# Kernel tuning notes

Hardware: AMD Instinct MI355X
Metric: run time of the kernel (lower is better)

Reference implementation:

```python
import jax, jax.numpy as jnp
import numpy as np

B, D = 8192, 4096  # batch, flattened feature dim
RATIO = 0.2


def setup_inputs() -> dict:
    key = jax.random.key(0)
    x = jax.random.normal(key, (B, D), dtype=jnp.float32)
    k = int(np.ceil(RATIO * D))  # 820, static for lax.top_k
    return {"x": x, "k": k}


def reference(x, k):
    # k-Winners-Take-All: per row, keep values >= k-th largest, zero the rest.
    kth_largest = jax.lax.top_k(x, k)[0][:, -1]  # [B]
    return jnp.where(x < kth_largest[:, None], 0.0, x)
```

## Files before the change

### kernel.cpp

```cpp
#include <hip/hip_runtime.h>
#include <stdint.h>

#define D_DIM   4096
#define THREADS 256

__device__ __forceinline__ int wave_reduce_add(int v) {
    #pragma unroll
    for (int m = 32; m >= 1; m >>= 1) v += __shfl_xor(v, m, 64);
    return v;
}
__device__ __forceinline__ uint32_t wave_reduce_min(uint32_t v) {
    #pragma unroll
    for (int m = 32; m >= 1; m >>= 1) {
        uint32_t o = (uint32_t)__shfl_xor((int)v, m, 64);
        v = (o < v) ? o : v;
    }
    return v;
}
__device__ __forceinline__ uint32_t wave_reduce_max(uint32_t v) {
    #pragma unroll
    for (int m = 32; m >= 1; m >>= 1) {
        uint32_t o = (uint32_t)__shfl_xor((int)v, m, 64);
        v = (o > v) ? o : v;
    }
    return v;
}

__global__ __launch_bounds__(THREADS, 4)
void kwta_kernel(const float* __restrict__ x, const int* __restrict__ kptr,
                 float* __restrict__ out) {
    const int row  = blockIdx.x;
    const int t    = threadIdx.x;
    const int wid  = t >> 6;
    const int lane = t & 63;
    const size_t base = (size_t)row * D_DIM;
    const float4* __restrict__ xr = reinterpret_cast<const float4*>(x + base);
    float4* __restrict__ orow     = reinterpret_cast<float4*>(out + base);
    const int k = kptr[0];

    uint32_t u[16];
    #pragma unroll
    for (int j = 0; j < 4; ++j) {
        float4 v = xr[t + j * THREADS];
        uint32_t b[4] = { __float_as_uint(v.x), __float_as_uint(v.y),
                          __float_as_uint(v.z), __float_as_uint(v.w) };
        #pragma unroll
        for (int e = 0; e < 4; ++e) {
            uint32_t f = b[e];
            u[j * 4 + e] = ((int32_t)f < 0) ? ~f : (f | 0x80000000u);
        }
    }

    uint32_t mn = 0xFFFFFFFFu, mx = 0u;
    #pragma unroll
    for (int e = 0; e < 16; ++e) {
        mn = (u[e] < mn) ? u[e] : mn;
        mx = (u[e] > mx) ? u[e] : mx;
    }
    mn = wave_reduce_min(mn);
    mx = wave_reduce_max(mx);

    __shared__ uint32_t smn[4], smx[4];
    __shared__ int      scnt[4];
    if (lane == 0) { smn[wid] = mn; smx[wid] = mx; }
    __syncthreads();
    uint32_t lo = smn[0]; lo = (smn[1] < lo) ? smn[1] : lo;
             lo = (smn[2] < lo) ? smn[2] : lo; lo = (smn[3] < lo) ? smn[3] : lo;
    uint32_t hi = smx[0]; hi = (smx[1] > hi) ? smx[1] : hi;
             hi = (smx[2] > hi) ? smx[2] : hi; hi = (smx[3] > hi) ? smx[3] : hi;

    #pragma unroll 1
    while (lo < hi) {
        uint32_t diff = hi - lo;
        uint32_t mid  = lo + (diff >> 1) + (diff & 1u);
        int c = 0;
        #pragma unroll
        for (int e = 0; e < 16; ++e) c += (u[e] >= mid) ? 1 : 0;
        c = wave_reduce_add(c);
        __syncthreads();
        if (lane == 0) scnt[wid] = c;
        __syncthreads();
        int total = scnt[0] + scnt[1] + scnt[2] + scnt[3];
        if (total >= k) lo = mid; else hi = mid - 1u;
    }

    const uint32_t thr = lo;
    #pragma unroll
    for (int j = 0; j < 4; ++j) {
        float4 o;
        float* po = &o.x;
        #pragma unroll
        for (int e = 0; e < 4; ++e) {
            uint32_t uu = u[j * 4 + e];
            uint32_t f  = (uu & 0x80000000u) ? (uu ^ 0x80000000u) : ~uu;
            po[e] = (uu >= thr) ? __uint_as_float(f) : 0.0f;
        }
        orow[t + j * THREADS] = o;
    }
}

extern "C" void kernel_launch(void* const* d_in, const int* in_sizes, int n_in,
                              void* d_out, int out_size, void* d_ws, size_t ws_size,
                              hipStream_t stream) {
    const float* x    = (const float*)d_in[0];
    const int*   kptr = (const int*)d_in[1];
    float*       out  = (float*)d_out;
    const int rows = out_size / D_DIM;
    kwta_kernel<<<rows, THREADS, 0, stream>>>(x, kptr, out);
}
```

Baseline: 261.2 us.

## Assign one wavefront per row and count with ballot/popcount instead of block barriers

Each 64-lane wavefront now owns a full row (64 values per lane), so the per-row binary-search threshold is found without shared memory or __syncthreads. The per-iteration count uses ballot plus popcount on each element instead of a shuffle reduction followed by two block barriers. This removes the roughly 32 barrier round-trips per row. In exchange, register use rises to 64 values per lane, which may lower occupancy, and there are 64 ballots per search step.

```diff
diff --git a/kernel.cpp b/kernel.cpp
--- a/kernel.cpp
+++ b/kernel.cpp
@@ -1,14 +1,9 @@
 #include <hip/hip_runtime.h>
 #include <stdint.h>
 
-#define D_DIM   4096
-#define THREADS 256
+#define D_DIM          4096
+#define ROWS_PER_BLOCK 4
 
-__device__ __forceinline__ int wave_reduce_add(int v) {
-    #pragma unroll
-    for (int m = 32; m >= 1; m >>= 1) v += __shfl_xor(v, m, 64);
-    return v;
-}
 __device__ __forceinline__ uint32_t wave_reduce_min(uint32_t v) {
     #pragma unroll
     for (int m = 32; m >= 1; m >>= 1) {
@@ -26,22 +21,21 @@
     return v;
 }
 
-__global__ __launch_bounds__(THREADS, 4)
+__global__ __launch_bounds__(256)
 void kwta_kernel(const float* __restrict__ x, const int* __restrict__ kptr,
                  float* __restrict__ out) {
-    const int row  = blockIdx.x;
-    const int t    = threadIdx.x;
-    const int wid  = t >> 6;
-    const int lane = t & 63;
+    const int wid  = threadIdx.x >> 6;
+    const int lane = threadIdx.x & 63;
+    const int row  = blockIdx.x * ROWS_PER_BLOCK + wid;
     const size_t base = (size_t)row * D_DIM;
     const float4* __restrict__ xr = reinterpret_cast<const float4*>(x + base);
     float4* __restrict__ orow     = reinterpret_cast<float4*>(out + base);
     const int k = kptr[0];
 
-    uint32_t u[16];
+    uint32_t u[64];
     #pragma unroll
-    for (int j = 0; j < 4; ++j) {
-        float4 v = xr[t + j * THREADS];
+    for (int j = 0; j < 16; ++j) {
+        float4 v = xr[lane + j * 64];
         uint32_t b[4] = { __float_as_uint(v.x), __float_as_uint(v.y),
                           __float_as_uint(v.z), __float_as_uint(v.w) };
         #pragma unroll
@@ -53,21 +47,12 @@
 
     uint32_t mn = 0xFFFFFFFFu, mx = 0u;
     #pragma unroll
-    for (int e = 0; e < 16; ++e) {
+    for (int e = 0; e < 64; ++e) {
         mn = (u[e] < mn) ? u[e] : mn;
         mx = (u[e] > mx) ? u[e] : mx;
     }
-    mn = wave_reduce_min(mn);
-    mx = wave_reduce_max(mx);
-
-    __shared__ uint32_t smn[4], smx[4];
-    __shared__ int      scnt[4];
-    if (lane == 0) { smn[wid] = mn; smx[wid] = mx; }
-    __syncthreads();
-    uint32_t lo = smn[0]; lo = (smn[1] < lo) ? smn[1] : lo;
-             lo = (smn[2] < lo) ? smn[2] : lo; lo = (smn[3] < lo) ? smn[3] : lo;
-    uint32_t hi = smx[0]; hi = (smx[1] > hi) ? smx[1] : hi;
-             hi = (smx[2] > hi) ? smx[2] : hi; hi = (smx[3] > hi) ? smx[3] : hi;
+    uint32_t lo = wave_reduce_min(mn);
+    uint32_t hi = wave_reduce_max(mx);
 
     #pragma unroll 1
     while (lo < hi) {
@@ -75,18 +60,14 @@
         uint32_t mid  = lo + (diff >> 1) + (diff & 1u);
         int c = 0;
         #pragma unroll
-        for (int e = 0; e < 16; ++e) c += (u[e] >= mid) ? 1 : 0;
-        c = wave_reduce_add(c);
-        __syncthreads();
-        if (lane == 0) scnt[wid] = c;
-        __syncthreads();
-        int total = scnt[0] + scnt[1] + scnt[2] + scnt[3];
-        if (total >= k) lo = mid; else hi = mid - 1u;
+        for (int e = 0; e < 64; ++e)
+            c += (int)__popcll(__ballot(u[e] >= mid));
+        if (c >= k) lo = mid; else hi = mid - 1u;
     }
 
     const uint32_t thr = lo;
     #pragma unroll
-    for (int j = 0; j < 4; ++j) {
+    for (int j = 0; j < 16; ++j) {
         float4 o;
         float* po = &o.x;
         #pragma unroll
@@ -95,7 +76,7 @@
             uint32_t f  = (uu & 0x80000000u) ? (uu ^ 0x80000000u) : ~uu;
             po[e] = (uu >= thr) ? __uint_as_float(f) : 0.0f;
         }
-        orow[t + j * THREADS] = o;
+        orow[lane + j * 64] = o;
     }
 }
 
@@ -105,6 +86,7 @@
     const float* x    = (const float*)d_in[0];
     const int*   kptr = (const int*)d_in[1];
     float*       out  = (float*)d_out;
-    const int rows = out_size / D_DIM;
-    kwta_kernel<<<rows, THREADS, 0, stream>>>(x, kptr, out);
+    const int rows   = out_size / D_DIM;
+    const int blocks = rows / ROWS_PER_BLOCK;
+    kwta_kernel<<<blocks, 256, 0, stream>>>(x, kptr, out);
 }
```

New measurement: 270.6 us. 1.04x slower.

## Replace bisection threshold search with 4-pass 8-bit radix select via LDS histograms

Applied to the files above, without the earlier changes.

Replaces the up-to-32-iteration binary search over the order-preserving uint keys with a 4-level radix select. Each level builds a 256-bin shared-memory histogram of the next 8 bits for elements matching the current prefix, then uses a wave suffix scan to locate the bin containing the k-th largest. This cuts the number of block-wide reductions and barriers from about 32 to 4, at the cost of LDS atomics that may contend when many values share a bin. The launch bounds are also raised to request more resident blocks per CU.

```diff
diff --git a/kernel.cpp b/kernel.cpp
--- a/kernel.cpp
+++ b/kernel.cpp
@@ -4,39 +4,18 @@
 #define D_DIM   4096
 #define THREADS 256
 
-__device__ __forceinline__ int wave_reduce_add(int v) {
-    #pragma unroll
-    for (int m = 32; m >= 1; m >>= 1) v += __shfl_xor(v, m, 64);
-    return v;
-}
-__device__ __forceinline__ uint32_t wave_reduce_min(uint32_t v) {
-    #pragma unroll
-    for (int m = 32; m >= 1; m >>= 1) {
-        uint32_t o = (uint32_t)__shfl_xor((int)v, m, 64);
-        v = (o < v) ? o : v;
-    }
-    return v;
-}
-__device__ __forceinline__ uint32_t wave_reduce_max(uint32_t v) {
-    #pragma unroll
-    for (int m = 32; m >= 1; m >>= 1) {
-        uint32_t o = (uint32_t)__shfl_xor((int)v, m, 64);
-        v = (o > v) ? o : v;
-    }
-    return v;
-}
-
-__global__ __launch_bounds__(THREADS, 4)
+__global__ __launch_bounds__(THREADS, 8)
 void kwta_kernel(const float* __restrict__ x, const int* __restrict__ kptr,
                  float* __restrict__ out) {
+    __shared__ uint32_t hist[2][256];
+
+    const int t    = threadIdx.x;
+    const int lane = t & 63;
     const int row  = blockIdx.x;
-    const int t    = threadIdx.x;
-    const int wid  = t >> 6;
-    const int lane = t & 63;
     const size_t base = (size_t)row * D_DIM;
     const float4* __restrict__ xr = reinterpret_cast<const float4*>(x + base);
     float4* __restrict__ orow     = reinterpret_cast<float4*>(out + base);
-    const int k = kptr[0];
+    int k = kptr[0];
 
     uint32_t u[16];
     #pragma unroll
@@ -51,40 +30,60 @@
         }
     }
 
-    uint32_t mn = 0xFFFFFFFFu, mx = 0u;
+    uint32_t pref = 0, maskHi = 0;
+    int shift = 24;
     #pragma unroll
-    for (int e = 0; e < 16; ++e) {
-        mn = (u[e] < mn) ? u[e] : mn;
-        mx = (u[e] > mx) ? u[e] : mx;
-    }
-    mn = wave_reduce_min(mn);
-    mx = wave_reduce_max(mx);
+    for (int L = 0; L < 4; ++L) {
+        uint32_t* __restrict__ h = hist[L & 1];
+        h[t] = 0;
+        __syncthreads();
+        #pragma unroll
+        for (int e = 0; e < 16; ++e) {
+            if ((u[e] & maskHi) == pref)
+                atomicAdd(&h[(u[e] >> shift) & 0xFFu], 1u);
+        }
+        __syncthreads();
 
-    __shared__ uint32_t smn[4], smx[4];
-    __shared__ int      scnt[4];
-    if (lane == 0) { smn[wid] = mn; smx[wid] = mx; }
-    __syncthreads();
-    uint32_t lo = smn[0]; lo = (smn[1] < lo) ? smn[1] : lo;
-             lo = (smn[2] < lo) ? smn[2] : lo; lo = (smn[3] < lo) ? smn[3] : lo;
-    uint32_t hi = smx[0]; hi = (smx[1] > hi) ? smx[1] : hi;
-             hi = (smx[2] > hi) ? smx[2] : hi; hi = (smx[3] > hi) ? smx[3] : hi;
-
-    #pragma unroll 1
-    while (lo < hi) {
-        uint32_t diff = hi - lo;
-        uint32_t mid  = lo + (diff >> 1) + (diff & 1u);
-        int c = 0;
+        uint4 hv = *reinterpret_cast<const uint4*>(&h[lane * 4]);
+        uint32_t s3 = hv.w;
+        uint32_t s2 = hv.z + s3;
+        uint32_t s1 = hv.y + s2;
+        uint32_t s0 = hv.x + s1;
+        uint32_t W = s0;
         #pragma unroll
-        for (int e = 0; e < 16; ++e) c += (u[e] >= mid) ? 1 : 0;
-        c = wave_reduce_add(c);
-        __syncthreads();
-        if (lane == 0) scnt[wid] = c;
-        __syncthreads();
-        int total = scnt[0] + scnt[1] + scnt[2] + scnt[3];
-        if (total >= k) lo = mid; else hi = mid - 1u;
+        for (int m = 1; m <= 32; m <<= 1) {
+            uint32_t o = (uint32_t)__shfl_down((int)W, m, 64);
+            if (lane + m < 64) W += o;
+        }
+        const uint32_t above = W - s0;
+        const uint32_t S0 = above + s0, S1 = above + s1,
+                       S2 = above + s2, S3 = above + s3;
+        const uint32_t uk = (uint32_t)k;
+        int bi = -1;
+        if      (S3 >= uk) bi = 3;
+        else if (S2 >= uk) bi = 2;
+        else if (S1 >= uk) bi = 1;
+        else if (S0 >= uk) bi = 0;
+        uint32_t key = 0;
+        if (bi >= 0) {
+            uint32_t b  = (uint32_t)(lane * 4 + bi);
+            uint32_t Sb = (bi == 0) ? S0 : (bi == 1) ? S1 : (bi == 2) ? S2 : S3;
+            uint32_t hb = (bi == 0) ? hv.x : (bi == 1) ? hv.y : (bi == 2) ? hv.z : hv.w;
+            key = (b << 24) | (Sb - hb);
+        }
+        #pragma unroll
+        for (int m = 32; m >= 1; m >>= 1) {
+            uint32_t o = (uint32_t)__shfl_xor((int)key, m, 64);
+            key = (o > key) ? o : key;
+        }
+        const uint32_t b = key >> 24;
+        k -= (int)(key & 0xFFFFFFu);
+        pref   |= b << shift;
+        maskHi |= 0xFFu << shift;
+        shift  -= 8;
     }
 
-    const uint32_t thr = lo;
+    const uint32_t thr = pref;
     #pragma unroll
     for (int j = 0; j < 4; ++j) {
         float4 o;
```

Result: faster. 235.3 us (-9.9%).

## Replace block-wide bisection with histogram radix select plus candidate compaction

Applied to the files above, without the earlier changes.

Swaps the 32-step block-wide binary search, which needs two barriers per step, for a 4096-bin shared-memory histogram on the top 12 key bits. A block-wide prefix scan over the bins finds the bin that holds the k-th value. Elements in that bin are compacted into shared memory, and every wave then bisects the low 20 bits redundantly using ballot counts, with no block barriers. It adds shared-memory atomics and 16KB of LDS per block, and raises the launch-bounds occupancy hint to 8.

```diff
diff --git a/kernel.cpp b/kernel.cpp
--- a/kernel.cpp
+++ b/kernel.cpp
@@ -3,36 +3,19 @@
 
 #define D_DIM   4096
 #define THREADS 256
+#define NBINS   4096
 
-__device__ __forceinline__ int wave_reduce_add(int v) {
-    #pragma unroll
-    for (int m = 32; m >= 1; m >>= 1) v += __shfl_xor(v, m, 64);
-    return v;
-}
-__device__ __forceinline__ uint32_t wave_reduce_min(uint32_t v) {
-    #pragma unroll
-    for (int m = 32; m >= 1; m >>= 1) {
-        uint32_t o = (uint32_t)__shfl_xor((int)v, m, 64);
-        v = (o < v) ? o : v;
-    }
-    return v;
-}
-__device__ __forceinline__ uint32_t wave_reduce_max(uint32_t v) {
-    #pragma unroll
-    for (int m = 32; m >= 1; m >>= 1) {
-        uint32_t o = (uint32_t)__shfl_xor((int)v, m, 64);
-        v = (o > v) ? o : v;
-    }
-    return v;
-}
-
-__global__ __launch_bounds__(THREADS, 4)
+__global__ __launch_bounds__(THREADS, 8)
 void kwta_kernel(const float* __restrict__ x, const int* __restrict__ kptr,
                  float* __restrict__ out) {
-    const int row  = blockIdx.x;
+    __shared__ uint32_t hist[NBINS];
+    __shared__ uint32_t wtot[4];
+    __shared__ int pub_bin, pub_kp, ns;
+
     const int t    = threadIdx.x;
     const int wid  = t >> 6;
     const int lane = t & 63;
+    const int row  = blockIdx.x;
     const size_t base = (size_t)row * D_DIM;
     const float4* __restrict__ xr = reinterpret_cast<const float4*>(x + base);
     float4* __restrict__ orow     = reinterpret_cast<float4*>(out + base);
@@ -51,40 +34,103 @@
         }
     }
 
-    uint32_t mn = 0xFFFFFFFFu, mx = 0u;
+    #pragma unroll
+    for (int j = 0; j < 4; ++j)
+        reinterpret_cast<uint4*>(hist)[t + j * THREADS] = make_uint4(0, 0, 0, 0);
+    if (t == 0) ns = 0;
+    __syncthreads();
+
+    #pragma unroll
+    for (int e = 0; e < 16; ++e)
+        atomicAdd(&hist[u[e] >> 20], 1u);
+    __syncthreads();
+
+    uint32_t h[16];
+    #pragma unroll
+    for (int j = 0; j < 4; ++j) {
+        uint4 hv = reinterpret_cast<const uint4*>(hist)[4 * t + j];
+        h[4 * j + 0] = hv.x; h[4 * j + 1] = hv.y;
+        h[4 * j + 2] = hv.z; h[4 * j + 3] = hv.w;
+    }
+    uint32_t T = 0;
+    #pragma unroll
+    for (int i = 0; i < 16; ++i) T += h[i];
+    uint32_t W = T;
+    #pragma unroll
+    for (int m = 1; m <= 32; m <<= 1) {
+        uint32_t o = (uint32_t)__shfl_down((int)W, m, 64);
+        if (lane + m < 64) W += o;
+    }
+    if (lane == 0) wtot[wid] = W;
+    __syncthreads();
+    uint32_t above = W - T;
+    #pragma unroll
+    for (int w = 0; w < 4; ++w)
+        if (w > wid) above += wtot[w];
+    if (above < (uint32_t)k && (uint32_t)k <= above + T) {
+        uint32_t cum = above;
+        #pragma unroll
+        for (int i = 15; i >= 0; --i) {
+            cum += h[i];
+            if (cum >= (uint32_t)k) {
+                pub_bin = 16 * t + i;
+                pub_kp  = k - (int)(cum - h[i]);
+                break;
+            }
+        }
+    }
+    __syncthreads();
+    const uint32_t bin = (uint32_t)pub_bin;
+    const int kp = pub_kp;
+
     #pragma unroll
     for (int e = 0; e < 16; ++e) {
-        mn = (u[e] < mn) ? u[e] : mn;
-        mx = (u[e] > mx) ? u[e] : mx;
+        const bool m = (u[e] >> 20) == bin;
+        unsigned long long mk = __ballot(m);
+        int cnt = (int)__popcll(mk);
+        int bs = 0;
+        if (lane == 0 && cnt) bs = atomicAdd(&ns, cnt);
+        bs = __shfl(bs, 0, 64);
+        if (m) {
+            int pos = bs + (int)__popcll(mk & ((1ull << lane) - 1ull));
+            hist[pos] = u[e];
+        }
     }
-    mn = wave_reduce_min(mn);
-    mx = wave_reduce_max(mx);
+    __syncthreads();
+    const int N = ns;
 
-    __shared__ uint32_t smn[4], smx[4];
-    __shared__ int      scnt[4];
-    if (lane == 0) { smn[wid] = mn; smx[wid] = mx; }
-    __syncthreads();
-    uint32_t lo = smn[0]; lo = (smn[1] < lo) ? smn[1] : lo;
-             lo = (smn[2] < lo) ? smn[2] : lo; lo = (smn[3] < lo) ? smn[3] : lo;
-    uint32_t hi = smx[0]; hi = (smx[1] > hi) ? smx[1] : hi;
-             hi = (smx[2] > hi) ? smx[2] : hi; hi = (smx[3] > hi) ? smx[3] : hi;
+    uint32_t lo = 0, hi = 0xFFFFFu;
+    if (N <= 256) {
+        uint32_t v[4];
+        #pragma unroll
+        for (int c = 0; c < 4; ++c) {
+            int idx = 64 * c + lane;
+            v[c] = (idx < N) ? (hist[idx] & 0xFFFFFu) : 0u;
+        }
+        #pragma unroll 1
+        while (lo < hi) {
+            uint32_t mid = lo + ((hi - lo + 1u) >> 1);
+            int c = 0;
+            #pragma unroll
+            for (int j = 0; j < 4; ++j)
+                c += (int)__popcll(__ballot(v[j] >= mid));
+            if (c >= kp) lo = mid; else hi = mid - 1u;
+        }
+    } else {
+        #pragma unroll 1
+        while (lo < hi) {
+            uint32_t mid = lo + ((hi - lo + 1u) >> 1);
+            int c = 0;
+            for (int cb = 0; cb < N; cb += 64) {
+                uint32_t vv = 0;
+                if (cb + lane < N) vv = hist[cb + lane] & 0xFFFFFu;
+                c += (int)__popcll(__ballot(vv >= mid));
+            }
+            if (c >= kp) lo = mid; else hi = mid - 1u;
+        }
+    }
+    const uint32_t thr = (bin << 20) | lo;
 
-    #pragma unroll 1
-    while (lo < hi) {
-        uint32_t diff = hi - lo;
-        uint32_t mid  = lo + (diff >> 1) + (diff & 1u);
-        int c = 0;
-        #pragma unroll
-        for (int e = 0; e < 16; ++e) c += (u[e] >= mid) ? 1 : 0;
-        c = wave_reduce_add(c);
-        __syncthreads();
-        if (lane == 0) scnt[wid] = c;
-        __syncthreads();
-        int total = scnt[0] + scnt[1] + scnt[2] + scnt[3];
-        if (total >= k) lo = mid; else hi = mid - 1u;
-    }
-
-    const uint32_t thr = lo;
     #pragma unroll
     for (int j = 0; j < 4; ++j) {
         float4 o;
```

New measurement: 232.0 us. -11.2%, faster.
